# Performance work log

Hardware: AMD Instinct MI355X
Metric: run time of the kernel (lower is better)

## Reference

```python
import jax, jax.numpy as jnp
import numpy as np

STATE_DIM = 128
HIDDEN = 128
NUM_HEADS = 16
TEMPERATURE = 1.0
NEG_INF = float('-inf')


def setup_inputs() -> dict:
    key = jax.random.key(0)
    ks = jax.random.split(key, 8)
    B, S = 2, 512
    state_embeddings = jax.random.normal(ks[0], (B, S, STATE_DIM), dtype=jnp.float32)
    mask = jnp.ones((B, S, S), dtype=bool)
    # MLP params (Linear stores [in, out] here; we apply x @ W + b)
    W1 = jax.random.normal(ks[1], (2 * STATE_DIM, HIDDEN), dtype=jnp.float32) / np.sqrt(2 * STATE_DIM)
    b1 = jnp.zeros((HIDDEN,), dtype=jnp.float32)
    W2 = jax.random.normal(ks[2], (HIDDEN, HIDDEN), dtype=jnp.float32) / np.sqrt(HIDDEN)
    b2 = jnp.zeros((HIDDEN,), dtype=jnp.float32)
    W3 = jax.random.normal(ks[3], (HIDDEN, NUM_HEADS), dtype=jnp.float32) / np.sqrt(HIDDEN)
    b3 = jnp.zeros((NUM_HEADS,), dtype=jnp.float32)
    head_temperatures = jnp.ones((NUM_HEADS,), dtype=jnp.float32) * TEMPERATURE
    return {
        'state_embeddings': state_embeddings,
        'mask': mask,
        'W1': W1, 'b1': b1, 'W2': W2, 'b2': b2, 'W3': W3, 'b3': b3,
        'head_temperatures': head_temperatures,
    }


def reference(state_embeddings, mask, W1, b1, W2, b2, W3, b3, head_temperatures):
    # Split first Linear: cat([x_i, x_j]) @ W1 == x_i @ W1a + x_j @ W1b
    # This avoids materializing the [B, S, S, 2*state_dim] pairwise concat
    # while computing identical math.
    W1a, W1b = W1[:STATE_DIM], W1[STATE_DIM:]
    hi = jnp.einsum('bsd,dh->bsh', state_embeddings, W1a) + b1  # [B,S,H]
    hj = jnp.einsum('bsd,dh->bsh', state_embeddings, W1b)       # [B,S,H]
    h = jax.nn.relu(hi[:, :, None, :] + hj[:, None, :, :])       # [B,S,S,H]
    h = jax.nn.relu(jnp.einsum('bijh,hk->bijk', h, W2) + b2)     # [B,S,S,H]
    comp = jnp.einsum('bijh,hn->bijn', h, W3) + b3               # [B,S,S,heads]
    bias = jnp.transpose(comp, (0, 3, 1, 2))                     # [B,heads,S,S]
    bias = bias * head_temperatures[None, :, None, None]
    bias = jnp.where(mask[:, None, :, :], bias, NEG_INF)
    return bias
```

## Files before the change

### kernel.cpp

```cpp
#include <hip/hip_runtime.h>
#include <math.h>

typedef _Float16 half8 __attribute__((ext_vector_type(8)));
typedef _Float16 half4v __attribute__((ext_vector_type(4)));
typedef float floatx4 __attribute__((ext_vector_type(4)));

__global__ __launch_bounds__(128) void prep_kernel(
    const float* __restrict__ E,
    const float* __restrict__ W1,
    const float* __restrict__ b1,
    const float* __restrict__ W2,
    const float* __restrict__ W3,
    float* __restrict__ hi,
    _Float16* __restrict__ hjh,
    _Float16* __restrict__ W2frag,
    _Float16* __restrict__ W3frag)
{
    const int blk = blockIdx.x;
    const int t = threadIdx.x;
    if (blk < 1024) {
        __shared__ float sE[128];
        sE[t] = E[blk*128 + t];
        __syncthreads();
        float ai = b1[t];
        float aj = 0.f;
        #pragma unroll 8
        for (int d = 0; d < 128; ++d) {
            float e = sE[d];
            ai = fmaf(e, W1[d*128 + t], ai);
            aj = fmaf(e, W1[(128+d)*128 + t], aj);
        }
        hi[blk*128 + t] = ai;
        hjh[blk*128 + t] = (_Float16)aj;
    } else if (blk == 1024) {
        for (int e = t; e < 16384; e += 128) {
            int q = e & 7, l = (e >> 3) & 63, g = e >> 9;
            int wr = g >> 4, nt = (g >> 2) & 3, ks = g & 3;
            int row = 64*wr + 16*nt + (l & 15);
            int k = ks*32 + (l >> 4)*8 + q;
            W2frag[e] = (_Float16)W2[k*128 + row];
        }
    } else {
        for (int e = t; e < 2048; e += 128) {
            int q = e & 7, l = (e >> 3) & 63, ks = e >> 9;
            int k = ks*32 + (l >> 4)*8 + q;
            W3frag[e] = (_Float16)W3[k*16 + (l & 15)];
        }
    }
}

__global__ __launch_bounds__(256, 2) void main_kernel(
    const float* __restrict__ hi,
    const _Float16* __restrict__ hjh,
    const _Float16* __restrict__ W2frag,
    const _Float16* __restrict__ W3frag,
    const float* __restrict__ b2,
    const float* __restrict__ b3,
    const float* __restrict__ temps,
    const int* __restrict__ mask,
    float* __restrict__ out)
{
    constexpr int PADH = 136;
    __shared__ _Float16 sH[128 * PADH];
    __shared__ float sHi[128];
    __shared__ float sB2[128];

    const int tid = threadIdx.x;
    const int bid = blockIdx.x;
    const int b  = bid >> 11;
    const int i  = (bid >> 2) & 511;
    const int j0 = (bid & 3) << 7;

    const int lane = tid & 63;
    const int wave = tid >> 6;
    const int wr = wave >> 1;
    const int wc = wave & 1;
    const int lr = lane & 15;
    const int lq = lane >> 4;

    half8 aW[4][4];
    const half8* w2v = (const half8*)W2frag;
    #pragma unroll
    for (int nt = 0; nt < 4; ++nt)
        #pragma unroll
        for (int ks = 0; ks < 4; ++ks)
            aW[nt][ks] = w2v[((wr*4 + nt)*4 + ks)*64 + lane];

    if (tid < 128) {
        sHi[tid] = hi[(b*512 + i)*128 + tid];
        sB2[tid] = b2[tid];
    }
    __syncthreads();

    {
        const int row = tid >> 1;
        const _Float16* hjrow = &hjh[(b*512 + j0 + row)*128];
        #pragma unroll
        for (int kk = 0; kk < 8; ++kk) {
            const int kb = (tid & 1)*8 + kk*16;
            half8 hv = *(const half8*)&hjrow[kb];
            float4 c0 = *(const float4*)&sHi[kb];
            float4 c1 = *(const float4*)&sHi[kb + 4];
            half8 o;
            o[0] = (_Float16)fmaxf((float)hv[0] + c0.x, 0.f);
            o[1] = (_Float16)fmaxf((float)hv[1] + c0.y, 0.f);
            o[2] = (_Float16)fmaxf((float)hv[2] + c0.z, 0.f);
            o[3] = (_Float16)fmaxf((float)hv[3] + c0.w, 0.f);
            o[4] = (_Float16)fmaxf((float)hv[4] + c1.x, 0.f);
            o[5] = (_Float16)fmaxf((float)hv[5] + c1.y, 0.f);
            o[6] = (_Float16)fmaxf((float)hv[6] + c1.z, 0.f);
            o[7] = (_Float16)fmaxf((float)hv[7] + c1.w, 0.f);
            *(half8*)&sH[row*PADH + kb] = o;
        }
    }
    __syncthreads();

    floatx4 acc[4][4] = {};
    #pragma unroll
    for (int ks = 0; ks < 4; ++ks) {
        const int k0 = ks*32;
        half8 bF[4];
        #pragma unroll
        for (int mt = 0; mt < 4; ++mt)
            bF[mt] = *(const half8*)&sH[(64*wc + 16*mt + lr)*PADH + k0 + lq*8];
        #pragma unroll
        for (int nt = 0; nt < 4; ++nt)
            #pragma unroll
            for (int mt = 0; mt < 4; ++mt)
                acc[nt][mt] = __builtin_amdgcn_mfma_f32_16x16x32_f16(
                    aW[nt][ks], bF[mt], acc[nt][mt], 0, 0, 0);
    }
    __syncthreads();

    #pragma unroll
    for (int nt = 0; nt < 4; ++nt) {
        const int nb = 64*wr + 16*nt + 4*lq;
        float4 bv = *(const float4*)&sB2[nb];
        #pragma unroll
        for (int mt = 0; mt < 4; ++mt) {
            const int m = 64*wc + 16*mt + lr;
            floatx4 v = acc[nt][mt];
            half4v o;
            o[0] = (_Float16)fmaxf(v[0] + bv.x, 0.f);
            o[1] = (_Float16)fmaxf(v[1] + bv.y, 0.f);
            o[2] = (_Float16)fmaxf(v[2] + bv.z, 0.f);
            o[3] = (_Float16)fmaxf(v[3] + bv.w, 0.f);
            *(half4v*)&sH[m*PADH + nb] = o;
        }
    }
    __syncthreads();

    half8 bW[4];
    const half8* w3v = (const half8*)W3frag;
    #pragma unroll
    for (int ks = 0; ks < 4; ++ks) bW[ks] = w3v[ks*64 + lane];

    floatx4 acc2[2] = {};
    const int m0 = 32*wave;
    #pragma unroll
    for (int ks = 0; ks < 4; ++ks) {
        const int k0 = ks*32;
        half8 a0 = *(const half8*)&sH[(m0 + lr)*PADH + k0 + lq*8];
        half8 a1 = *(const half8*)&sH[(m0 + 16 + lr)*PADH + k0 + lq*8];
        acc2[0] = __builtin_amdgcn_mfma_f32_16x16x32_f16(a0, bW[ks], acc2[0], 0, 0, 0);
        acc2[1] = __builtin_amdgcn_mfma_f32_16x16x32_f16(a1, bW[ks], acc2[1], 0, 0, 0);
    }

    const int n2 = lr;
    const float tempv = temps[n2];
    const float b3v = b3[n2];
    const int* mrow = &mask[(b*512 + i)*512];
    float* outp = &out[(((b*16 + n2)*512) + i)*512];
    #pragma unroll
    for (int mt2 = 0; mt2 < 2; ++mt2) {
        const int j = j0 + m0 + 16*mt2 + 4*lq;
        floatx4 v = acc2[mt2];
        int4 mk = *(const int4*)&mrow[j];
        float4 res;
        res.x = mk.x ? (v[0] + b3v)*tempv : -INFINITY;
        res.y = mk.y ? (v[1] + b3v)*tempv : -INFINITY;
        res.z = mk.z ? (v[2] + b3v)*tempv : -INFINITY;
        res.w = mk.w ? (v[3] + b3v)*tempv : -INFINITY;
        *(float4*)&outp[j] = res;
    }
}

extern "C" void kernel_launch(void* const* d_in, const int* in_sizes, int n_in,
                              void* d_out, int out_size, void* d_ws, size_t ws_size,
                              hipStream_t stream)
{
    const float* E     = (const float*)d_in[0];
    const int* mask    = (const int*)d_in[1];
    const float* W1    = (const float*)d_in[2];
    const float* b1    = (const float*)d_in[3];
    const float* W2    = (const float*)d_in[4];
    const float* b2    = (const float*)d_in[5];
    const float* W3    = (const float*)d_in[6];
    const float* b3    = (const float*)d_in[7];
    const float* temps = (const float*)d_in[8];

    char* ws = (char*)d_ws;
    float*    hi  = (float*)ws;
    _Float16* hjh = (_Float16*)(ws + 524288);
    _Float16* W2f = (_Float16*)(ws + 524288 + 262144);
    _Float16* W3f = W2f + 16384;

    prep_kernel<<<1026, 128, 0, stream>>>(E, W1, b1, W2, W3, hi, hjh, W2f, W3f);
    main_kernel<<<4096, 256, 0, stream>>>(hi, hjh, W2f, W3f, b2, b3, temps, mask,
                                          (float*)d_out);
}
```

Measured before the change: 126.2 us.

## Fuse layer-1 ReLU into MFMA operand loads and cut shared memory staging

The main kernel no longer stages the relu(hi+hj) tile in shared memory. Each wave now loads hj rows straight from global memory as fp16 and applies the add plus ReLU in packed half precision right before the MFMA. W2 and W3 fragments are loaded per k-step instead of all at once, which lowers register pressure, and the occupancy hint rises from 2 to 3 blocks per CU. The prep kernel splits the hi and hj products across 256 threads and stores hi in fp16. In exchange, the hi+hj sum is now computed in fp16, and more redundant global/L2 loads are issued, since each hj row is fetched by both wave rows.

Result: slower. 142.6 us (+13.0%).

```diff
diff --git a/kernel.cpp b/kernel.cpp
--- a/kernel.cpp
+++ b/kernel.cpp
@@ -5,13 +5,13 @@
 typedef _Float16 half4v __attribute__((ext_vector_type(4)));
 typedef float floatx4 __attribute__((ext_vector_type(4)));
 
-__global__ __launch_bounds__(128) void prep_kernel(
+__global__ __launch_bounds__(256) void prep_kernel(
     const float* __restrict__ E,
     const float* __restrict__ W1,
     const float* __restrict__ b1,
     const float* __restrict__ W2,
     const float* __restrict__ W3,
-    float* __restrict__ hi,
+    _Float16* __restrict__ hih,
     _Float16* __restrict__ hjh,
     _Float16* __restrict__ W2frag,
     _Float16* __restrict__ W3frag)
@@ -20,20 +20,19 @@
     const int t = threadIdx.x;
     if (blk < 1024) {
         __shared__ float sE[128];
-        sE[t] = E[blk*128 + t];
+        if (t < 128) sE[t] = E[blk*128 + t];
         __syncthreads();
-        float ai = b1[t];
-        float aj = 0.f;
+        const int half = t >> 7;
+        const int k = t & 127;
+        float acc = half ? 0.f : b1[k];
+        const float* w1col = &W1[half*128*128 + k];
         #pragma unroll 8
-        for (int d = 0; d < 128; ++d) {
-            float e = sE[d];
-            ai = fmaf(e, W1[d*128 + t], ai);
-            aj = fmaf(e, W1[(128+d)*128 + t], aj);
-        }
-        hi[blk*128 + t] = ai;
-        hjh[blk*128 + t] = (_Float16)aj;
+        for (int d = 0; d < 128; ++d)
+            acc = fmaf(sE[d], w1col[d*128], acc);
+        if (half == 0) hih[blk*128 + k] = (_Float16)acc;
+        else           hjh[blk*128 + k] = (_Float16)acc;
     } else if (blk == 1024) {
-        for (int e = t; e < 16384; e += 128) {
+        for (int e = t; e < 16384; e += 256) {
             int q = e & 7, l = (e >> 3) & 63, g = e >> 9;
             int wr = g >> 4, nt = (g >> 2) & 3, ks = g & 3;
             int row = 64*wr + 16*nt + (l & 15);
@@ -41,7 +40,7 @@
             W2frag[e] = (_Float16)W2[k*128 + row];
         }
     } else {
-        for (int e = t; e < 2048; e += 128) {
+        for (int e = t; e < 2048; e += 256) {
             int q = e & 7, l = (e >> 3) & 63, ks = e >> 9;
             int k = ks*32 + (l >> 4)*8 + q;
             W3frag[e] = (_Float16)W3[k*16 + (l & 15)];
@@ -49,8 +48,8 @@
     }
 }
 
-__global__ __launch_bounds__(256, 2) void main_kernel(
-    const float* __restrict__ hi,
+__global__ __launch_bounds__(256, 3) void main_kernel(
+    const _Float16* __restrict__ hih,
     const _Float16* __restrict__ hjh,
     const _Float16* __restrict__ W2frag,
     const _Float16* __restrict__ W3frag,
@@ -62,8 +61,6 @@
 {
     constexpr int PADH = 136;
     __shared__ _Float16 sH[128 * PADH];
-    __shared__ float sHi[128];
-    __shared__ float sB2[128];
 
     const int tid = threadIdx.x;
     const int bid = blockIdx.x;
@@ -78,64 +75,39 @@
     const int lr = lane & 15;
     const int lq = lane >> 4;
 
-    half8 aW[4][4];
+    const half8 zero8 = {};
+    const _Float16* hirow = &hih[(b*512 + i)*128];
+    const _Float16* hjbase = &hjh[(b*512 + j0)*128];
     const half8* w2v = (const half8*)W2frag;
-    #pragma unroll
-    for (int nt = 0; nt < 4; ++nt)
-        #pragma unroll
-        for (int ks = 0; ks < 4; ++ks)
-            aW[nt][ks] = w2v[((wr*4 + nt)*4 + ks)*64 + lane];
-
-    if (tid < 128) {
-        sHi[tid] = hi[(b*512 + i)*128 + tid];
-        sB2[tid] = b2[tid];
-    }
-    __syncthreads();
-
-    {
-        const int row = tid >> 1;
-        const _Float16* hjrow = &hjh[(b*512 + j0 + row)*128];
-        #pragma unroll
-        for (int kk = 0; kk < 8; ++kk) {
-            const int kb = (tid & 1)*8 + kk*16;
-            half8 hv = *(const half8*)&hjrow[kb];
-            float4 c0 = *(const float4*)&sHi[kb];
-            float4 c1 = *(const float4*)&sHi[kb + 4];
-            half8 o;
-            o[0] = (_Float16)fmaxf((float)hv[0] + c0.x, 0.f);
-            o[1] = (_Float16)fmaxf((float)hv[1] + c0.y, 0.f);
-            o[2] = (_Float16)fmaxf((float)hv[2] + c0.z, 0.f);
-            o[3] = (_Float16)fmaxf((float)hv[3] + c0.w, 0.f);
-            o[4] = (_Float16)fmaxf((float)hv[4] + c1.x, 0.f);
-            o[5] = (_Float16)fmaxf((float)hv[5] + c1.y, 0.f);
-            o[6] = (_Float16)fmaxf((float)hv[6] + c1.z, 0.f);
-            o[7] = (_Float16)fmaxf((float)hv[7] + c1.w, 0.f);
-            *(half8*)&sH[row*PADH + kb] = o;
-        }
-    }
-    __syncthreads();
 
     floatx4 acc[4][4] = {};
     #pragma unroll
     for (int ks = 0; ks < 4; ++ks) {
-        const int k0 = ks*32;
+        const int kb = ks*32 + lq*8;
+        half8 aW[4];
+        #pragma unroll
+        for (int nt = 0; nt < 4; ++nt)
+            aW[nt] = w2v[((wr*4 + nt)*4 + ks)*64 + lane];
+        const half8 hi8 = *(const half8*)&hirow[kb];
         half8 bF[4];
         #pragma unroll
-        for (int mt = 0; mt < 4; ++mt)
-            bF[mt] = *(const half8*)&sH[(64*wc + 16*mt + lr)*PADH + k0 + lq*8];
+        for (int mt = 0; mt < 4; ++mt) {
+            const int m = 64*wc + 16*mt + lr;
+            half8 hj8 = *(const half8*)&hjbase[m*128 + kb];
+            bF[mt] = __builtin_elementwise_max(hi8 + hj8, zero8);
+        }
         #pragma unroll
         for (int nt = 0; nt < 4; ++nt)
             #pragma unroll
             for (int mt = 0; mt < 4; ++mt)
                 acc[nt][mt] = __builtin_amdgcn_mfma_f32_16x16x32_f16(
-                    aW[nt][ks], bF[mt], acc[nt][mt], 0, 0, 0);
+                    aW[nt], bF[mt], acc[nt][mt], 0, 0, 0);
     }
-    __syncthreads();
 
     #pragma unroll
     for (int nt = 0; nt < 4; ++nt) {
         const int nb = 64*wr + 16*nt + 4*lq;
-        float4 bv = *(const float4*)&sB2[nb];
+        const float4 bv = *(const float4*)&b2[nb];
         #pragma unroll
         for (int mt = 0; mt < 4; ++mt) {
             const int m = 64*wc + 16*mt + lr;
@@ -150,20 +122,17 @@
     }
     __syncthreads();
 
-    half8 bW[4];
     const half8* w3v = (const half8*)W3frag;
-    #pragma unroll
-    for (int ks = 0; ks < 4; ++ks) bW[ks] = w3v[ks*64 + lane];
-
     floatx4 acc2[2] = {};
     const int m0 = 32*wave;
     #pragma unroll
     for (int ks = 0; ks < 4; ++ks) {
-        const int k0 = ks*32;
-        half8 a0 = *(const half8*)&sH[(m0 + lr)*PADH + k0 + lq*8];
-        half8 a1 = *(const half8*)&sH[(m0 + 16 + lr)*PADH + k0 + lq*8];
-        acc2[0] = __builtin_amdgcn_mfma_f32_16x16x32_f16(a0, bW[ks], acc2[0], 0, 0, 0);
-        acc2[1] = __builtin_amdgcn_mfma_f32_16x16x32_f16(a1, bW[ks], acc2[1], 0, 0, 0);
+        const int k0 = ks*32 + lq*8;
+        half8 bW = w3v[ks*64 + lane];
+        half8 a0 = *(const half8*)&sH[(m0 + lr)*PADH + k0];
+        half8 a1 = *(const half8*)&sH[(m0 + 16 + lr)*PADH + k0];
+        acc2[0] = __builtin_amdgcn_mfma_f32_16x16x32_f16(a0, bW, acc2[0], 0, 0, 0);
+        acc2[1] = __builtin_amdgcn_mfma_f32_16x16x32_f16(a1, bW, acc2[1], 0, 0, 0);
     }
 
     const int n2 = lr;
@@ -200,12 +169,12 @@
     const float* temps = (const float*)d_in[8];
 
     char* ws = (char*)d_ws;
-    float*    hi  = (float*)ws;
-    _Float16* hjh = (_Float16*)(ws + 524288);
-    _Float16* W2f = (_Float16*)(ws + 524288 + 262144);
+    _Float16* hih = (_Float16*)ws;
+    _Float16* hjh = (_Float16*)(ws + 262144);
+    _Float16* W2f = (_Float16*)(ws + 524288);
     _Float16* W3f = W2f + 16384;
 
-    prep_kernel<<<1026, 128, 0, stream>>>(E, W1, b1, W2, W3, hi, hjh, W2f, W3f);
-    main_kernel<<<4096, 256, 0, stream>>>(hi, hjh, W2f, W3f, b2, b3, temps, mask,
+    prep_kernel<<<1026, 256, 0, stream>>>(E, W1, b1, W2, W3, hih, hjh, W2f, W3f);
+    main_kernel<<<4096, 256, 0, stream>>>(hih, hjh, W2f, W3f, b2, b3, temps, mask,
                                           (float*)d_out);
 }
```
